# Kernel tuning notes

Measured on AMD Instinct MI355X. Metric: run time of the kernel, lower is better.

The kernel has to match this reference:

```python
import jax, jax.numpy as jnp
import numpy as np

NEG_SLOPE = 0.2


def setup_inputs() -> dict:
    key = jax.random.key(0)
    k1, k2, k3, k4, k5, k6 = jax.random.split(key, 6)
    N, E, IN, OUT = 100000, 1600000, 256, 32
    feat = jax.random.normal(k1, (N, IN), dtype=jnp.float32)
    W = jax.random.normal(k2, (IN, OUT), dtype=jnp.float32) * (1.0 / np.sqrt(IN))
    attn_l = jax.random.normal(k3, (OUT,), dtype=jnp.float32) * 0.1
    attn_r = jax.random.normal(k4, (OUT,), dtype=jnp.float32) * 0.1
    bias = jnp.zeros((OUT,), dtype=jnp.float32)
    src = jax.random.randint(k5, (E,), 0, N, dtype=jnp.int32)
    dst = jax.random.randint(k6, (E,), 0, N, dtype=jnp.int32)
    return {"feat": feat, "W": W, "attn_l": attn_l, "attn_r": attn_r,
            "bias": bias, "src": src, "dst": dst}


def reference(feat, W, attn_l, attn_r, bias, src, dst):
    N = feat.shape[0]
    # dense projection: [N, in] @ [in, out] -> [N, out]
    h = feat @ W
    el = h @ attn_l  # [N]
    er = h @ attn_r  # [N]
    # per-edge raw score: el[u] + er[v] for edge u->v
    e = el[src] + er[dst]  # [E]
    e = jnp.where(e > 0, e, NEG_SLOPE * e)  # leaky relu
    # edge softmax grouped by destination node (numerically stable)
    m = jax.ops.segment_max(e, dst, num_segments=N)  # [N], -inf for isolated nodes
    m = jax.lax.stop_gradient(m)
    ex = jnp.exp(e - m[dst])  # [E]
    denom = jax.ops.segment_sum(ex, dst, num_segments=N)  # [N]
    alpha = ex / denom[dst]  # [E]
    # weighted aggregation (sparse SpMM): sum_{u->v} alpha_uv * h[u]
    rst = jax.ops.segment_sum(h[src] * alpha[:, None], dst, num_segments=N)  # [N, out]
    return rst + bias
```

## Files before the change

### kernel.cpp

```cpp
#include <hip/hip_runtime.h>
#include <hip/hip_bf16.h>
#include <math.h>

#define NEG_SLOPE 0.2f
#define BUCK_BITS 6
#define BUCK_NODES 64
#define CAP 1408
#define FB 128
#define SRC_MASK 0x1FFFFFF

typedef __bf16 bf16x8 __attribute__((ext_vector_type(8)));
typedef float  f32x4  __attribute__((ext_vector_type(4)));

__global__ void pack_w(const float* __restrict__ W, __bf16* __restrict__ Whi) {
    int idx = blockIdx.x * blockDim.x + threadIdx.x;
    if (idx >= 8192) return;
    int j = idx & 7, lane = (idx >> 3) & 63, nt = (idx >> 9) & 1, kt = idx >> 10;
    int q = lane >> 4, c = lane & 15;
    int k = kt * 32 + q * 8 + j;
    int n = nt * 16 + c;
    Whi[idx] = (__bf16)W[k * 32 + n];
}

__global__ __launch_bounds__(256) void gemm_h(const float* __restrict__ feat,
                                              const __bf16* __restrict__ Whi,
                                              const float* __restrict__ attn_l,
                                              const float* __restrict__ attn_r,
                                              float* __restrict__ h,
                                              float* __restrict__ el,
                                              float* __restrict__ er,
                                              int N, int Ntiles) {
    __shared__ bf16x8 sB[1024];
    int tid = threadIdx.x;
    for (int i = tid; i < 1024; i += 256) sB[i] = ((const bf16x8*)Whi)[i];
    __syncthreads();

    int wid  = blockIdx.x * 4 + (tid >> 6);
    int lane = tid & 63;
    if (wid >= Ntiles) return;

    int c = lane & 15, q = lane >> 4;
    int row = wid * 16 + c;
    if (row >= N) row = N - 1;
    const float* A = feat + (size_t)row * 256 + q * 8;

    f32x4 acc0 = {0.f, 0.f, 0.f, 0.f};
    f32x4 acc1 = {0.f, 0.f, 0.f, 0.f};
#pragma unroll
    for (int kt = 0; kt < 8; kt++) {
        f32x4 a0 = *(const f32x4*)(A + kt * 32);
        f32x4 a1 = *(const f32x4*)(A + kt * 32 + 4);
        bf16x8 ah, al;
#pragma unroll
        for (int j = 0; j < 4; j++) {
            __bf16 h0 = (__bf16)a0[j];
            __bf16 h1 = (__bf16)a1[j];
            ah[j]     = h0;
            ah[j + 4] = h1;
            al[j]     = (__bf16)(a0[j] - (float)h0);
            al[j + 4] = (__bf16)(a1[j] - (float)h1);
        }
        bf16x8 bh0 = sB[(kt * 2 + 0) * 64 + lane];
        bf16x8 bh1 = sB[(kt * 2 + 1) * 64 + lane];
        acc0 = __builtin_amdgcn_mfma_f32_16x16x32_bf16(ah, bh0, acc0, 0, 0, 0);
        acc0 = __builtin_amdgcn_mfma_f32_16x16x32_bf16(al, bh0, acc0, 0, 0, 0);
        acc1 = __builtin_amdgcn_mfma_f32_16x16x32_bf16(ah, bh1, acc1, 0, 0, 0);
        acc1 = __builtin_amdgcn_mfma_f32_16x16x32_bf16(al, bh1, acc1, 0, 0, 0);
    }

    float alc  = attn_l[c],      arc  = attn_r[c];
    float alc2 = attn_l[c + 16], arc2 = attn_r[c + 16];
#pragma unroll
    for (int r = 0; r < 4; r++) {
        int m = wid * 16 + q * 4 + r;
        if (m < N) {
            h[(size_t)m * 32 + c]      = acc0[r];
            h[(size_t)m * 32 + 16 + c] = acc1[r];
        }
        float pl = acc0[r] * alc + acc1[r] * alc2;
        float pr = acc0[r] * arc + acc1[r] * arc2;
#pragma unroll
        for (int off = 8; off >= 1; off >>= 1) {
            pl += __shfl_xor(pl, off);
            pr += __shfl_xor(pr, off);
        }
        if (c == 0 && m < N) { el[m] = pl; er[m] = pr; }
    }
}

__global__ __launch_bounds__(512) void bin_fill(const int* __restrict__ src,
                                                const int* __restrict__ dst,
                                                unsigned int* __restrict__ cursor,
                                                unsigned int* __restrict__ binned,
                                                int E, int NBUK, int batch) {
    __shared__ unsigned int hist[1600];
    __shared__ unsigned int cbase[1600];
    int tid = threadIdx.x;
    int b0 = blockIdx.x * batch;
    int b1 = min(b0 + batch, E);
    for (int i = tid; i < NBUK; i += 512) hist[i] = 0;
    __syncthreads();
    for (int i = b0 + tid; i < b1; i += 512)
        atomicAdd(&hist[((unsigned)dst[i]) >> BUCK_BITS], 1u);
    __syncthreads();
    for (int i = tid; i < NBUK; i += 512) {
        unsigned c = hist[i];
        cbase[i] = c ? atomicAdd(&cursor[i], c) : 0u;
        hist[i] = 0;
    }
    __syncthreads();
    for (int i = b0 + tid; i < b1; i += 512) {
        int d = dst[i];
        unsigned b = ((unsigned)d) >> BUCK_BITS;
        unsigned r = atomicAdd(&hist[b], 1u);
        unsigned pos = cbase[b] + r;
        if (pos < CAP)
            binned[(size_t)b * CAP + pos] =
                (((unsigned)(d & (BUCK_NODES - 1))) << 25) | (unsigned)src[i];
    }
}

__global__ __launch_bounds__(256) void aggregate(const unsigned int* __restrict__ cursor,
                                                 const unsigned int* __restrict__ binned,
                                                 const float* __restrict__ el,
                                                 const float* __restrict__ er,
                                                 const float* __restrict__ h,
                                                 const float* __restrict__ bias,
                                                 float* __restrict__ out, int N) {
    __shared__ int          rec_s[CAP];
    __shared__ float        w_s[CAP];
    __shared__ unsigned int hist[BUCK_NODES];
    __shared__ int          off_s[BUCK_NODES + 1];
    __shared__ float        den[BUCK_NODES];
    __shared__ float        er_l[BUCK_NODES];

    int buck = blockIdx.x;
    int base = buck << BUCK_BITS;
    int nn = min(BUCK_NODES, N - base);
    int tid = threadIdx.x;

    int cnt = (int)min(cursor[buck], (unsigned)CAP);
    const unsigned int* eb = binned + (size_t)buck * CAP;

    if (tid < BUCK_NODES) {
        hist[tid] = 0;
        den[tid] = 0.f;
        er_l[tid] = (tid < nn) ? er[base + tid] : 0.f;
    }
    __syncthreads();

    unsigned int rl[6];
    int k = 0;
    for (int i = tid; i < cnt; i += 256) {
        unsigned r = eb[i];
        rl[k++] = r;
        atomicAdd(&hist[r >> 25], 1u);
    }
    __syncthreads();

    if (tid < 64) {
        int v = (int)hist[tid];
        int orig = v;
#pragma unroll
        for (int off = 1; off < 64; off <<= 1) {
            int x = __shfl_up(v, off);
            if (tid >= off) v += x;
        }
        off_s[tid] = v - orig;
        if (tid == 63) off_s[64] = v;
        hist[tid] = (unsigned)(v - orig);
    }
    __syncthreads();

    k = 0;
    for (int i = tid; i < cnt; i += 256) {
        unsigned r = rl[k++];
        int s = r & SRC_MASK;
        int d = r >> 25;
        float e = el[s] + er_l[d];
        e = (e > 0.f) ? e : NEG_SLOPE * e;
        float w = __expf(e);
        unsigned pos = atomicAdd(&hist[d], 1u);
        rec_s[pos] = s;
        w_s[pos] = w;
        atomicAdd(&den[d], w);
    }
    __syncthreads();

    int lane = tid & 63, wv = tid >> 6;
    int q = lane >> 4, t = lane & 15;
    float2 b2 = *(const float2*)&bias[t * 2];
    for (int n = wv; n < nn; n += 4) {
        float sm = den[n];
        int s0 = off_s[n], s1 = off_s[n + 1];
        float ax = 0.f, ay = 0.f;
        for (int j = s0 + q; j < s1; j += 4) {
            float w = w_s[j];
            int s = rec_s[j];
            float2 hv = *(const float2*)&h[(size_t)s * 32 + t * 2];
            ax += w * hv.x;
            ay += w * hv.y;
        }
        ax += __shfl_xor(ax, 16); ay += __shfl_xor(ay, 16);
        ax += __shfl_xor(ax, 32); ay += __shfl_xor(ay, 32);
        if (lane < 16) {
            float2 o;
            if (sm > 0.f) {
                float inv = 1.f / sm;
                o.x = ax * inv + b2.x;
                o.y = ay * inv + b2.y;
            } else {
                o = b2;
            }
            *(float2*)&out[(size_t)(base + n) * 32 + t * 2] = o;
        }
    }
}

static inline size_t align256(size_t x) { return (x + 255) & ~(size_t)255; }

extern "C" void kernel_launch(void* const* d_in, const int* in_sizes, int n_in,
                              void* d_out, int out_size, void* d_ws, size_t ws_size,
                              hipStream_t stream) {
    const float* feat   = (const float*)d_in[0];
    const float* W      = (const float*)d_in[1];
    const float* attn_l = (const float*)d_in[2];
    const float* attn_r = (const float*)d_in[3];
    const float* bias   = (const float*)d_in[4];
    const int* src = (const int*)d_in[5];
    const int* dst = (const int*)d_in[6];
    float* out = (float*)d_out;

    const int IN = 256;
    int N = in_sizes[0] / IN;
    int E = in_sizes[5];
    (void)n_in; (void)out_size; (void)ws_size;

    int Ntiles = (N + 15) / 16;
    int NBUK = (N + BUCK_NODES - 1) >> BUCK_BITS;
    int batch = (E + FB - 1) / FB;

    char* p = (char*)d_ws;
    float* h       = (float*)p; p += align256((size_t)N * 32 * 4);
    float* el      = (float*)p; p += align256((size_t)N * 4);
    float* er      = (float*)p; p += align256((size_t)N * 4);
    unsigned int* cursor = (unsigned int*)p; p += align256((size_t)1600 * 4);
    unsigned int* binned = (unsigned int*)p; p += align256((size_t)NBUK * CAP * 4);
    __bf16* Whi    = (__bf16*)p; p += align256((size_t)8192 * 2);

    pack_w<<<32, 256, 0, stream>>>(W, Whi);
    hipMemsetAsync(cursor, 0, (size_t)NBUK * 4, stream);
    gemm_h<<<(Ntiles + 3) / 4, 256, 0, stream>>>(feat, Whi, attn_l, attn_r,
                                                 h, el, er, N, Ntiles);
    bin_fill<<<FB, 512, 0, stream>>>(src, dst, cursor, binned, E, NBUK, batch);
    aggregate<<<NBUK, 256, 0, stream>>>(cursor, binned, el, er, h, bias, out, N);
}
```

Before: 279.5 us.

## Halve edge buckets, vectorize aggregation gathers, fold cursor reset into prep kernel

Destination buckets shrink from 64 to 32 nodes, with the per-bucket capacity and bin-fill histogram sizes adjusted to match. This doubles the number of aggregate blocks and cuts their shared-memory footprint, which should improve load balance and occupancy. The aggregation loop now has each lane gather a float4 of h, with 8 edges processed in parallel per node instead of 4. The cursor memset moves into the W-packing kernel to remove one launch, and the streaming reads of feat, src and dst become nontemporal loads. The risk is more bucket overhead and more cursor atomics in bin_fill, and any bucket holding more than 800 edges would silently drop edges.

```diff
diff --git a/kernel.cpp b/kernel.cpp
--- a/kernel.cpp
+++ b/kernel.cpp
@@ -3,17 +3,20 @@
 #include <math.h>
 
 #define NEG_SLOPE 0.2f
-#define BUCK_BITS 6
-#define BUCK_NODES 64
-#define CAP 1408
+#define BUCK_BITS 5
+#define BUCK_NODES 32
+#define CAP 800
 #define FB 128
 #define SRC_MASK 0x1FFFFFF
+#define NBUK_MAX 3200
 
 typedef __bf16 bf16x8 __attribute__((ext_vector_type(8)));
 typedef float  f32x4  __attribute__((ext_vector_type(4)));
 
-__global__ void pack_w(const float* __restrict__ W, __bf16* __restrict__ Whi) {
+__global__ void prep(const float* __restrict__ W, __bf16* __restrict__ Whi,
+                     unsigned int* __restrict__ cursor, int NBUK) {
     int idx = blockIdx.x * blockDim.x + threadIdx.x;
+    if (idx < NBUK) cursor[idx] = 0u;
     if (idx >= 8192) return;
     int j = idx & 7, lane = (idx >> 3) & 63, nt = (idx >> 9) & 1, kt = idx >> 10;
     int q = lane >> 4, c = lane & 15;
@@ -42,14 +45,14 @@
     int c = lane & 15, q = lane >> 4;
     int row = wid * 16 + c;
     if (row >= N) row = N - 1;
-    const float* A = feat + (size_t)row * 256 + q * 8;
+    const f32x4* A = (const f32x4*)(feat + (size_t)row * 256 + q * 8);
 
     f32x4 acc0 = {0.f, 0.f, 0.f, 0.f};
     f32x4 acc1 = {0.f, 0.f, 0.f, 0.f};
 #pragma unroll
     for (int kt = 0; kt < 8; kt++) {
-        f32x4 a0 = *(const f32x4*)(A + kt * 32);
-        f32x4 a1 = *(const f32x4*)(A + kt * 32 + 4);
+        f32x4 a0 = __builtin_nontemporal_load(A + kt * 8);
+        f32x4 a1 = __builtin_nontemporal_load(A + kt * 8 + 1);
         bf16x8 ah, al;
 #pragma unroll
         for (int j = 0; j < 4; j++) {
@@ -93,15 +96,17 @@
                                                 unsigned int* __restrict__ cursor,
                                                 unsigned int* __restrict__ binned,
                                                 int E, int NBUK, int batch) {
-    __shared__ unsigned int hist[1600];
-    __shared__ unsigned int cbase[1600];
+    __shared__ unsigned int hist[NBUK_MAX];
+    __shared__ unsigned int cbase[NBUK_MAX];
     int tid = threadIdx.x;
     int b0 = blockIdx.x * batch;
     int b1 = min(b0 + batch, E);
     for (int i = tid; i < NBUK; i += 512) hist[i] = 0;
     __syncthreads();
-    for (int i = b0 + tid; i < b1; i += 512)
-        atomicAdd(&hist[((unsigned)dst[i]) >> BUCK_BITS], 1u);
+    for (int i = b0 + tid; i < b1; i += 512) {
+        int d = __builtin_nontemporal_load(dst + i);
+        atomicAdd(&hist[((unsigned)d) >> BUCK_BITS], 1u);
+    }
     __syncthreads();
     for (int i = tid; i < NBUK; i += 512) {
         unsigned c = hist[i];
@@ -110,13 +115,14 @@
     }
     __syncthreads();
     for (int i = b0 + tid; i < b1; i += 512) {
-        int d = dst[i];
+        int d = __builtin_nontemporal_load(dst + i);
+        int s = __builtin_nontemporal_load(src + i);
         unsigned b = ((unsigned)d) >> BUCK_BITS;
         unsigned r = atomicAdd(&hist[b], 1u);
         unsigned pos = cbase[b] + r;
         if (pos < CAP)
             binned[(size_t)b * CAP + pos] =
-                (((unsigned)(d & (BUCK_NODES - 1))) << 25) | (unsigned)src[i];
+                (((unsigned)(d & (BUCK_NODES - 1))) << 25) | (unsigned)s;
     }
 }
 
@@ -149,7 +155,7 @@
     }
     __syncthreads();
 
-    unsigned int rl[6];
+    unsigned int rl[4];
     int k = 0;
     for (int i = tid; i < cnt; i += 256) {
         unsigned r = eb[i];
@@ -158,16 +164,16 @@
     }
     __syncthreads();
 
-    if (tid < 64) {
+    if (tid < BUCK_NODES) {
         int v = (int)hist[tid];
         int orig = v;
 #pragma unroll
-        for (int off = 1; off < 64; off <<= 1) {
-            int x = __shfl_up(v, off);
+        for (int off = 1; off < BUCK_NODES; off <<= 1) {
+            int x = __shfl_up(v, off, 64);
             if (tid >= off) v += x;
         }
         off_s[tid] = v - orig;
-        if (tid == 63) off_s[64] = v;
+        if (tid == BUCK_NODES - 1) off_s[BUCK_NODES] = v;
         hist[tid] = (unsigned)(v - orig);
     }
     __syncthreads();
@@ -188,31 +194,40 @@
     __syncthreads();
 
     int lane = tid & 63, wv = tid >> 6;
-    int q = lane >> 4, t = lane & 15;
-    float2 b2 = *(const float2*)&bias[t * 2];
+    int oct = lane >> 3, t = lane & 7;
+    f32x4 b4 = *(const f32x4*)&bias[t * 4];
     for (int n = wv; n < nn; n += 4) {
         float sm = den[n];
         int s0 = off_s[n], s1 = off_s[n + 1];
-        float ax = 0.f, ay = 0.f;
-        for (int j = s0 + q; j < s1; j += 4) {
+        f32x4 acc = {0.f, 0.f, 0.f, 0.f};
+        for (int j = s0 + oct; j < s1; j += 8) {
             float w = w_s[j];
             int s = rec_s[j];
-            float2 hv = *(const float2*)&h[(size_t)s * 32 + t * 2];
-            ax += w * hv.x;
-            ay += w * hv.y;
-        }
-        ax += __shfl_xor(ax, 16); ay += __shfl_xor(ay, 16);
-        ax += __shfl_xor(ax, 32); ay += __shfl_xor(ay, 32);
-        if (lane < 16) {
-            float2 o;
+            f32x4 hv = *(const f32x4*)&h[(size_t)s * 32 + t * 4];
+            acc[0] += w * hv[0];
+            acc[1] += w * hv[1];
+            acc[2] += w * hv[2];
+            acc[3] += w * hv[3];
+        }
+#pragma unroll
+        for (int off = 8; off <= 32; off <<= 1) {
+            acc[0] += __shfl_xor(acc[0], off);
+            acc[1] += __shfl_xor(acc[1], off);
+            acc[2] += __shfl_xor(acc[2], off);
+            acc[3] += __shfl_xor(acc[3], off);
+        }
+        if (lane < 8) {
+            f32x4 o;
             if (sm > 0.f) {
                 float inv = 1.f / sm;
-                o.x = ax * inv + b2.x;
-                o.y = ay * inv + b2.y;
+                o[0] = acc[0] * inv + b4[0];
+                o[1] = acc[1] * inv + b4[1];
+                o[2] = acc[2] * inv + b4[2];
+                o[3] = acc[3] * inv + b4[3];
             } else {
-                o = b2;
+                o = b4;
             }
-            *(float2*)&out[(size_t)(base + n) * 32 + t * 2] = o;
+            *(f32x4*)&out[(size_t)(base + n) * 32 + t * 4] = o;
         }
     }
 }
@@ -244,12 +259,11 @@
     float* h       = (float*)p; p += align256((size_t)N * 32 * 4);
     float* el      = (float*)p; p += align256((size_t)N * 4);
     float* er      = (float*)p; p += align256((size_t)N * 4);
-    unsigned int* cursor = (unsigned int*)p; p += align256((size_t)1600 * 4);
+    unsigned int* cursor = (unsigned int*)p; p += align256((size_t)NBUK_MAX * 4);
     unsigned int* binned = (unsigned int*)p; p += align256((size_t)NBUK * CAP * 4);
     __bf16* Whi    = (__bf16*)p; p += align256((size_t)8192 * 2);
 
-    pack_w<<<32, 256, 0, stream>>>(W, Whi);
-    hipMemsetAsync(cursor, 0, (size_t)NBUK * 4, stream);
+    prep<<<33, 256, 0, stream>>>(W, Whi, cursor, NBUK);
     gemm_h<<<(Ntiles + 3) / 4, 256, 0, stream>>>(feat, Whi, attn_l, attn_r,
                                                  h, el, er, N, Ntiles);
     bin_fill<<<FB, 512, 0, stream>>>(src, dst, cursor, binned, E, NBUK, batch);
```

New measurement: 267.7 us. -4.2%, faster.
